# Performance work log

Hardware: AMD Instinct MI355X
Metric: run time of the kernel (lower is better)

## Reference

```python
import jax, jax.numpy as jnp
import numpy as np

B, L, S, DIM, H, DH, DFF = 2, 2048, 2048, 1024, 16, 64, 4096
EPS = 1e-6


def _ln(x, w, b):
    m = jnp.mean(x, axis=-1, keepdims=True)
    v = jnp.mean(jnp.square(x - m), axis=-1, keepdims=True)
    return (x - m) / jnp.sqrt(v + EPS) * w + b


def _mha(q, k, v, mask):
    # q: [B,L,H*DH], k/v: [B,S,H*DH], mask broadcastable to [B,H,L,S], True = masked
    b, l, _ = q.shape
    s = k.shape[1]
    q = q.reshape(b, l, H, DH)
    k = k.reshape(b, s, H, DH)
    v = v.reshape(b, s, H, DH)
    scale = 1.0 / np.sqrt(DH).astype(np.float32)
    attn = jnp.einsum('blhd,bshd->bhls', q, k) * scale
    if mask is not None:
        attn = jnp.where(mask, -jnp.inf, attn)
    attn = jax.nn.softmax(attn, axis=-1)
    out = jnp.einsum('bhls,bshd->blhd', attn, v)
    return out.reshape(b, l, H * DH)


def setup_inputs() -> dict:
    key = jax.random.key(0)
    ks = jax.random.split(key, 12)
    std = 0.02
    inp = {
        'input': jax.random.normal(ks[0], (B, L, DIM), jnp.float32),
        'source': jax.random.normal(ks[1], (B, S, DIM), jnp.float32),
        # source mask: no source positions masked
        'source_mask': jnp.zeros((B, 1, 1, S), bool),
        # causal mask for self-attention (True above diagonal -> masked)
        'mask': jnp.triu(jnp.ones((L, L), bool), 1)[None, None],
        # self-attention
        'ln_self_w': jnp.ones((DIM,), jnp.float32),
        'ln_self_b': jnp.zeros((DIM,), jnp.float32),
        'w_qkv': std * jax.random.normal(ks[2], (DIM, 3 * DIM), jnp.float32),
        'b_qkv': jnp.zeros((3 * DIM,), jnp.float32),
        'w_so': std * jax.random.normal(ks[3], (DIM, DIM), jnp.float32),
        'b_so': jnp.zeros((DIM,), jnp.float32),
        # cross-attention
        'ln_cross_w': jnp.ones((DIM,), jnp.float32),
        'ln_cross_b': jnp.zeros((DIM,), jnp.float32),
        'w_q': std * jax.random.normal(ks[4], (DIM, DIM), jnp.float32),
        'b_q': jnp.zeros((DIM,), jnp.float32),
        'w_kv': std * jax.random.normal(ks[5], (DIM, 2 * DIM), jnp.float32),
        'b_kv': jnp.zeros((2 * DIM,), jnp.float32),
        'w_co': std * jax.random.normal(ks[6], (DIM, DIM), jnp.float32),
        'b_co': jnp.zeros((DIM,), jnp.float32),
        # MLP (1 layer)
        'ln_mlp_w': jnp.ones((DIM,), jnp.float32),
        'ln_mlp_b': jnp.zeros((DIM,), jnp.float32),
        'w_ff1': std * jax.random.normal(ks[7], (DIM, DFF), jnp.float32),
        'b_ff1': jnp.zeros((DFF,), jnp.float32),
        'w_ff2': std * jax.random.normal(ks[8], (DFF, DIM), jnp.float32),
        'b_ff2': jnp.zeros((DIM,), jnp.float32),
    }
    return inp


def reference(input, source, source_mask, mask,
              ln_self_w, ln_self_b, w_qkv, b_qkv, w_so, b_so,
              ln_cross_w, ln_cross_b, w_q, b_q, w_kv, b_kv, w_co, b_co,
              ln_mlp_w, ln_mlp_b, w_ff1, b_ff1, w_ff2, b_ff2):
    x = input
    # self-attention block (pre-LN)
    h = _ln(x, ln_self_w, ln_self_b)
    qkv = h @ w_qkv + b_qkv
    q, k, v = jnp.split(qkv, 3, axis=-1)
    sa = _mha(q, k, v, mask) @ w_so + b_so
    x = x + sa
    # cross-attention block (pre-LN)
    h = _ln(x, ln_cross_w, ln_cross_b)
    q = h @ w_q + b_q
    kv = source @ w_kv + b_kv
    k, v = jnp.split(kv, 2, axis=-1)
    ca = _mha(q, k, v, source_mask) @ w_co + b_co
    x = x + ca
    # feed-forward block (pre-LN), eval mode (no dropout/droppath)
    h = _ln(x, ln_mlp_w, ln_mlp_b)
    ff = jax.nn.gelu(h @ w_ff1 + b_ff1, approximate=False) @ w_ff2 + b_ff2
    x = x + ff
    return x
```

## Files before the change

### kernel.cpp

```cpp
#include <hip/hip_runtime.h>
#include <hip/hip_bf16.h>
#include <math.h>

typedef __bf16 bf16_t;
typedef __bf16 bf16x8 __attribute__((ext_vector_type(8)));
typedef __bf16 bf16x4 __attribute__((ext_vector_type(4)));
typedef float  f32x4  __attribute__((ext_vector_type(4)));

#define DIM   1024
#define NB    2
#define NL    2048
#define NS    2048
#define NH    16
#define NDH   64
#define NDFF  4096

template<int N> struct IC { static constexpr int value = N; };

#define DS_READ_B128(dst, addr) \
    asm volatile("ds_read_b128 %0, %1" : "=v"(dst) : "v"(addr))
#define LGKM0_FENCE() do { \
    asm volatile("s_waitcnt lgkmcnt(0)" ::: "memory"); \
    __builtin_amdgcn_sched_barrier(0); } while (0)

__device__ __forceinline__ bf16x8 ld_bf16x8(const bf16_t* p) {
    return *reinterpret_cast<const bf16x8*>(p);
}

__device__ __forceinline__ void gl_lds16(const bf16_t* g, bf16_t* l) {
    __builtin_amdgcn_global_load_lds(
        (const __attribute__((address_space(1))) void*)g,
        (__attribute__((address_space(3))) void*)l, 16, 0, 0);
}

__device__ __forceinline__ unsigned lds_u32(const bf16_t* p) {
    return (unsigned)(uintptr_t)(__attribute__((address_space(3))) const void*)p;
}

__global__ __launch_bounds__(256)
void wconv_kernel(const float* __restrict__ in, bf16_t* __restrict__ out, int K, int N)
{
    __shared__ float tile[32][33];
    int n0 = blockIdx.x * 32, k0 = blockIdx.y * 32;
    int tx = threadIdx.x & 31, ty = threadIdx.x >> 5;
    #pragma unroll
    for (int j = 0; j < 4; ++j)
        tile[ty + 8*j][tx] = in[(size_t)(k0 + ty + 8*j) * N + n0 + tx];
    __syncthreads();
    #pragma unroll
    for (int j = 0; j < 4; ++j)
        out[(size_t)(n0 + ty + 8*j) * K + k0 + tx] = (bf16_t)tile[tx][ty + 8*j];
}

__global__ __launch_bounds__(256)
void f2b_kernel(const float* __restrict__ in, bf16_t* __restrict__ out)
{
    size_t i = ((size_t)blockIdx.x * 256 + threadIdx.x) * 4;
    float4 v = *reinterpret_cast<const float4*>(in + i);
    bf16x4 o = { (bf16_t)v.x, (bf16_t)v.y, (bf16_t)v.z, (bf16_t)v.w };
    *reinterpret_cast<bf16x4*>(out + i) = o;
}

__global__ __launch_bounds__(256)
void ln_kernel(const float* __restrict__ x, const float* __restrict__ wgt,
               const float* __restrict__ bia, bf16_t* __restrict__ out)
{
    int row = blockIdx.x, tid = threadIdx.x;
    float4 xv = reinterpret_cast<const float4*>(x + (size_t)row * DIM)[tid];
    float s1 = xv.x + xv.y + xv.z + xv.w;
    float s2 = xv.x*xv.x + xv.y*xv.y + xv.z*xv.z + xv.w*xv.w;
    #pragma unroll
    for (int off = 32; off > 0; off >>= 1) {
        s1 += __shfl_xor(s1, off, 64);
        s2 += __shfl_xor(s2, off, 64);
    }
    __shared__ float red[8];
    int w = tid >> 6;
    if ((tid & 63) == 0) { red[w] = s1; red[w + 4] = s2; }
    __syncthreads();
    s1 = red[0] + red[1] + red[2] + red[3];
    s2 = red[4] + red[5] + red[6] + red[7];
    float mean = s1 * (1.0f / DIM);
    float var  = s2 * (1.0f / DIM) - mean * mean;
    float rstd = rsqrtf(var + 1e-6f);
    float4 wv = reinterpret_cast<const float4*>(wgt)[tid];
    float4 bv = reinterpret_cast<const float4*>(bia)[tid];
    bf16x4 o = { (bf16_t)((xv.x - mean) * rstd * wv.x + bv.x),
                 (bf16_t)((xv.y - mean) * rstd * wv.y + bv.y),
                 (bf16_t)((xv.z - mean) * rstd * wv.z + bv.z),
                 (bf16_t)((xv.w - mean) * rstd * wv.w + bv.w) };
    reinterpret_cast<bf16x4*>(out + (size_t)row * DIM)[tid] = o;
}

template<int EPI, int BM, int BN>
__global__ __launch_bounds__(256)
void gemm_kernel(const bf16_t* __restrict__ A, const bf16_t* __restrict__ BT,
                 const float* __restrict__ bias, const float* __restrict__ res,
                 void* __restrict__ out, int M, int N, int K)
{
    constexpr int WM = BM / 2, WN = BN / 2;
    constexpr int AM = WM / 16, AN = WN / 16;
    constexpr int ABE = (BM + BN) * 32;
    constexpr int LPS = (BM + BN) / 64;
    __shared__ __align__(16) bf16_t lds[3 * ABE];

    int tid = threadIdx.x;
    int lane = tid & 63, w = tid >> 6;
    int wr = w >> 1, wc = w & 1;
    int la = lane & 15, lg = lane >> 4;
    int m0 = blockIdx.y * BM, n0 = blockIdx.x * BN;

    f32x4 acc[AM][AN] = {};

    int sr = lane >> 2;
    int sc = ((lane & 3) ^ ((lane >> 3) & 3)) * 8;
    const bf16_t* Ap = A  + (size_t)(m0 + w * (BM / 4) + sr) * K + sc;
    const bf16_t* Bp = BT + (size_t)(n0 + w * (BN / 4) + sr) * K + sc;

    auto stage = [&](int t, int buf) {
        int k0 = t * 32;
        bf16_t* base = &lds[buf * ABE];
        #pragma unroll
        for (int i = 0; i < BM / 64; ++i)
            gl_lds16(Ap + ((size_t)i * 16) * K + k0, base + (w * (BM / 4) + i * 16) * 32);
        #pragma unroll
        for (int i = 0; i < BN / 64; ++i)
            gl_lds16(Bp + ((size_t)i * 16) * K + k0, base + (BM + w * (BN / 4) + i * 16) * 32);
    };

    unsigned ldsb = lds_u32(lds);
    unsigned kla = (la >> 1) & 3;
    unsigned a_base = ldsb + ((wr * WM + la) * 32 + (lg ^ kla) * 8) * 2;
    unsigned b_base = ldsb + (BM * 32 + (wc * WN + la) * 32 + (lg ^ kla) * 8) * 2;

    auto compute = [&](int buf) {
        unsigned dB = (unsigned)(buf * ABE * 2);
        bf16x8 af[AM], bfr[AN];
        #pragma unroll
        for (int mi = 0; mi < AM; ++mi)
            DS_READ_B128(af[mi], a_base + dB + mi * 1024);
        #pragma unroll
        for (int ni = 0; ni < AN; ++ni)
            DS_READ_B128(bfr[ni], b_base + dB + ni * 1024);
        LGKM0_FENCE();
        __builtin_amdgcn_s_setprio(1);
        #pragma unroll
        for (int mi = 0; mi < AM; ++mi)
            #pragma unroll
            for (int ni = 0; ni < AN; ++ni)
                acc[mi][ni] = __builtin_amdgcn_mfma_f32_16x16x32_bf16(
                                  af[mi], bfr[ni], acc[mi][ni], 0, 0, 0);
        __builtin_amdgcn_s_setprio(0);
    };

    int nt = K / 32;
    stage(0, 0);
    stage(1, 1);
    int buf = 0;
    for (int t = 0; t < nt - 1; ++t) {
        asm volatile("s_waitcnt vmcnt(%0)" :: "n"(LPS) : "memory");
        __builtin_amdgcn_s_barrier();
        __builtin_amdgcn_sched_barrier(0);
        if (t + 2 < nt) stage(t + 2, (t + 2) % 3);
        compute(buf);
        buf = (buf == 2) ? 0 : buf + 1;
    }
    asm volatile("s_waitcnt vmcnt(0)" ::: "memory");
    __builtin_amdgcn_s_barrier();
    __builtin_amdgcn_sched_barrier(0);
    compute(buf);

    #pragma unroll
    for (int mi = 0; mi < AM; ++mi) {
        #pragma unroll
        for (int ni = 0; ni < AN; ++ni) {
            #pragma unroll
            for (int i = 0; i < 4; ++i) {
                int row = m0 + wr * WM + mi * 16 + lg * 4 + i;
                int col = n0 + wc * WN + ni * 16 + la;
                float v = acc[mi][ni][i] + bias[col];
                if (EPI == 1) v = 0.5f * v * (1.0f + erff(v * 0.70710678118f));
                if (EPI == 2)
                    ((float*)out)[(size_t)row * N + col] = res[(size_t)row * N + col] + v;
                else
                    ((bf16_t*)out)[(size_t)row * N + col] = (bf16_t)v;
            }
        }
    }
}

template<int EPI>
__global__ __launch_bounds__(512, 2)
void gemm256d_kernel(const bf16_t* __restrict__ A, const bf16_t* __restrict__ BT,
                     const float* __restrict__ bias, void* __restrict__ out,
                     int M, int N, int K, int nbx)
{
    constexpr int DBE = 16384;
    __shared__ __align__(16) bf16_t lds[4 * DBE];

    int tid = threadIdx.x;
    int lane = tid & 63, w = tid >> 6;
    int wr = w >> 2, wc = w & 3;
    int la = lane & 15, lg = lane >> 4;

    int nwg = gridDim.x, bid = blockIdx.x;
    int swz = (bid & 7) * (nwg >> 3) + (bid >> 3);
    int m0 = (swz / nbx) * 256, n0 = (swz % nbx) * 256;

    f32x4 acc[8][4] = {};

    int sr = lane >> 2;
    int sc = ((lane & 3) ^ ((lane >> 3) & 3)) * 8;
    const bf16_t* Ap = A  + (size_t)(m0 + w * 16 + sr) * K + sc;
    const bf16_t* Bp = BT + (size_t)(n0 + w * 16 + sr) * K + sc;

    auto stage = [&](int t) {
        int k0 = t * 32;
        bf16_t* base = &lds[(t & 3) * DBE];
        gl_lds16(Ap + k0,                     base + w * 512);
        gl_lds16(Ap + (size_t)128 * K + k0,   base + 4096 + w * 512);
        gl_lds16(Bp + k0,                     base + 8192 + w * 512);
        gl_lds16(Bp + (size_t)128 * K + k0,   base + 12288 + w * 512);
    };

    unsigned ldsb = lds_u32(lds);
    unsigned kla = (la >> 1) & 3;
    unsigned a_base = ldsb + ((wr * 128 + la) * 32 + (lg ^ kla) * 8) * 2;
    unsigned b_base = ldsb + (8192 + (wc * 64 + la) * 32 + (lg ^ kla) * 8) * 2;

    int nt = K / 32;

    auto ktile = [&](int kt, auto vmc, bool do_stage) {
        if (do_stage) stage(kt + 3);
        asm volatile("s_waitcnt vmcnt(%0)" :: "n"(decltype(vmc)::value) : "memory");
        __builtin_amdgcn_s_barrier();
        __builtin_amdgcn_sched_barrier(0);
        unsigned dB = (unsigned)((kt & 3) * (DBE * 2));
        bf16x8 af[4], af2[4], bfr[4];
        #pragma unroll
        for (int mi = 0; mi < 4; ++mi)
            DS_READ_B128(af[mi], a_base + dB + mi * 1024);
        #pragma unroll
        for (int ni = 0; ni < 4; ++ni)
            DS_READ_B128(bfr[ni], b_base + dB + ni * 1024);
        LGKM0_FENCE();
        __builtin_amdgcn_s_setprio(1);
        #pragma unroll
        for (int mi = 0; mi < 4; ++mi)
            #pragma unroll
            for (int ni = 0; ni < 4; ++ni)
                acc[mi][ni] = __builtin_amdgcn_mfma_f32_16x16x32_bf16(
                                  af[mi], bfr[ni], acc[mi][ni], 0, 0, 0);
        __builtin_amdgcn_s_setprio(0);
        #pragma unroll
        for (int mi = 0; mi < 4; ++mi)
            DS_READ_B128(af2[mi], a_base + dB + (4 + mi) * 1024);
        LGKM0_FENCE();
        __builtin_amdgcn_s_setprio(1);
        #pragma unroll
        for (int mi = 0; mi < 4; ++mi)
            #pragma unroll
            for (int ni = 0; ni < 4; ++ni)
                acc[4 + mi][ni] = __builtin_amdgcn_mfma_f32_16x16x32_bf16(
                                      af2[mi], bfr[ni], acc[4 + mi][ni], 0, 0, 0);
        __builtin_amdgcn_s_setprio(0);
        __builtin_amdgcn_s_barrier();
        __builtin_amdgcn_sched_barrier(0);
    };

    stage(0); stage(1); stage(2);
    for (int kt = 0; kt < nt - 3; ++kt) ktile(kt, IC<12>{}, true);
    ktile(nt - 3, IC<8>{}, false);
    ktile(nt - 2, IC<4>{}, false);
    ktile(nt - 1, IC<0>{}, false);

    #pragma unroll
    for (int mi = 0; mi < 8; ++mi) {
        #pragma unroll
        for (int ni = 0; ni < 4; ++ni) {
            #pragma unroll
            for (int i = 0; i < 4; ++i) {
                int row = m0 + wr * 128 + mi * 16 + lg * 4 + i;
                int col = n0 + wc * 64 + ni * 16 + la;
                float v = acc[mi][ni][i] + bias[col];
                if (EPI == 1) v = 0.5f * v * (1.0f + erff(v * 0.70710678118f));
                ((bf16_t*)out)[(size_t)row * N + col] = (bf16_t)v;
            }
        }
    }
}

template<bool CAUSAL>
__global__ __launch_bounds__(256)
void attn_kernel(const bf16_t* __restrict__ Q, int qs,
                 const bf16_t* __restrict__ Kp, int ks,
                 const bf16_t* __restrict__ Vp, int vs,
                 bf16_t* __restrict__ O, int os, int L, int S)
{
    __shared__ __align__(16) bf16_t Ks[64 * 64];
    __shared__ __align__(16) bf16_t Vt[64 * 64];
    __shared__ __align__(16) bf16_t Ps[4][16 * 64];

    int tid = threadIdx.x, lane = tid & 63, w = tid >> 6;
    int la = lane & 15, lg = lane >> 4;
    int qtile = (CAUSAL ? (gridDim.x - 1 - blockIdx.x) : blockIdx.x) * 64;
    int b = blockIdx.y >> 4, h = blockIdx.y & 15;

    const bf16_t* qb = Q  + (size_t)(b * L) * qs + h * 64;
    const bf16_t* kb = Kp + (size_t)(b * S) * ks + h * 64;
    const bf16_t* vb = Vp + (size_t)(b * S) * vs + h * 64;
    bf16_t*       ob = O  + (size_t)(b * L) * os + h * 64;

    int qrow = qtile + w * 16 + la;
    bf16x8 qf0 = ld_bf16x8(qb + (size_t)qrow * qs + lg * 8);
    bf16x8 qf1 = ld_bf16x8(qb + (size_t)qrow * qs + 32 + lg * 8);
    #pragma unroll
    for (int j = 0; j < 8; ++j) { qf0[j] = qf0[j] * (bf16_t)0.125f; qf1[j] = qf1[j] * (bf16_t)0.125f; }

    f32x4 zero = {0.f, 0.f, 0.f, 0.f};
    f32x4 o[4];
    #pragma unroll
    for (int dt = 0; dt < 4; ++dt) o[dt] = zero;
    float lpart[4] = {0.f, 0.f, 0.f, 0.f};

    int rk  = tid >> 3;
    int ck8 = tid & 7;
    int sv0   = tid & 31;
    int dbase = (tid >> 5) * 8;
    int r7 = la & 7;

    int n_full = (CAUSAL ? qtile : S) / 64;
    int nit = n_full + (CAUSAL ? 1 : 0);

    bf16x8 kr0 = ld_bf16x8(kb + (size_t)rk * ks + ck8 * 8);
    bf16x8 kr1 = ld_bf16x8(kb + (size_t)(rk + 32) * ks + ck8 * 8);
    bf16x8 vr0 = ld_bf16x8(vb + (size_t)sv0 * vs + dbase);
    bf16x8 vr1 = ld_bf16x8(vb + (size_t)(sv0 + 32) * vs + dbase);

    for (int it = 0; it < nit; ++it) {
        int s0 = it * 64;
        bool diag = CAUSAL && (it == n_full);

        __syncthreads();
        *reinterpret_cast<bf16x8*>(&Ks[rk * 64 + ((ck8 ^ (rk & 7)) * 8)]) = kr0;
        *reinterpret_cast<bf16x8*>(&Ks[(rk + 32) * 64 + ((ck8 ^ (rk & 7)) * 8)]) = kr1;
        #pragma unroll
        for (int j = 0; j < 8; ++j) {
            Vt[(dbase + j) * 64 + (sv0 ^ (j << 3))]        = vr0[j];
            Vt[(dbase + j) * 64 + ((sv0 + 32) ^ (j << 3))] = vr1[j];
        }
        __syncthreads();

        if (it + 1 < nit) {
            int s1 = s0 + 64;
            kr0 = ld_bf16x8(kb + (size_t)(s1 + rk) * ks + ck8 * 8);
            kr1 = ld_bf16x8(kb + (size_t)(s1 + rk + 32) * ks + ck8 * 8);
            vr0 = ld_bf16x8(vb + (size_t)(s1 + sv0) * vs + dbase);
            vr1 = ld_bf16x8(vb + (size_t)(s1 + sv0 + 32) * vs + dbase);
        }

        f32x4 sf[4];
        #pragma unroll
        for (int ct = 0; ct < 4; ++ct) {
            const bf16_t* kr = &Ks[(ct * 16 + la) * 64];
            bf16x8 k0 = ld_bf16x8(kr + ((lg ^ r7) * 8));
            bf16x8 k1 = ld_bf16x8(kr + (((4 + lg) ^ r7) * 8));
            f32x4 z = zero;
            z = __builtin_amdgcn_mfma_f32_16x16x32_bf16(qf0, k0, z, 0, 0, 0);
            z = __builtin_amdgcn_mfma_f32_16x16x32_bf16(qf1, k1, z, 0, 0, 0);
            sf[ct] = z;
        }

        #pragma unroll
        for (int ct = 0; ct < 4; ++ct) {
            #pragma unroll
            for (int i = 0; i < 4; ++i) {
                float p = __expf(sf[ct][i]);
                if (diag) {
                    int sg = s0 + ct * 16 + la;
                    int qg = qtile + w * 16 + lg * 4 + i;
                    if (sg > qg) p = 0.f;
                }
                lpart[i] += p;
                int row = lg * 4 + i;
                Ps[w][row * 64 + ((ct * 16 + la) ^ ((row & 7) << 3))] = (bf16_t)p;
            }
        }

        bf16x8 pa0 = ld_bf16x8(&Ps[w][la * 64 + ((lg ^ r7) * 8)]);
        bf16x8 pa1 = ld_bf16x8(&Ps[w][la * 64 + (((4 + lg) ^ r7) * 8)]);
        #pragma unroll
        for (int dt = 0; dt < 4; ++dt) {
            const bf16_t* vr = &Vt[(dt * 16 + la) * 64];
            bf16x8 v0 = ld_bf16x8(vr + ((lg ^ r7) * 8));
            bf16x8 v1 = ld_bf16x8(vr + (((4 + lg) ^ r7) * 8));
            o[dt] = __builtin_amdgcn_mfma_f32_16x16x32_bf16(pa0, v0, o[dt], 0, 0, 0);
            o[dt] = __builtin_amdgcn_mfma_f32_16x16x32_bf16(pa1, v1, o[dt], 0, 0, 0);
        }
    }

    #pragma unroll
    for (int off = 1; off < 16; off <<= 1)
        #pragma unroll
        for (int i = 0; i < 4; ++i)
            lpart[i] += __shfl_xor(lpart[i], off, 64);

    #pragma unroll
    for (int dt = 0; dt < 4; ++dt)
        #pragma unroll
        for (int i = 0; i < 4; ++i) {
            int row = qtile + w * 16 + lg * 4 + i;
            float val = o[dt][i] / lpart[i];
            ob[(size_t)row * os + dt * 16 + la] = (bf16_t)val;
        }
}

extern "C" void kernel_launch(void* const* d_in, const int* in_sizes, int n_in,
                              void* d_out, int out_size, void* d_ws, size_t ws_size,
                              hipStream_t stream)
{
    const float* input     = (const float*)d_in[0];
    const float* source    = (const float*)d_in[1];
    const float* ln_self_w = (const float*)d_in[4];
    const float* ln_self_b = (const float*)d_in[5];
    const float* w_qkv     = (const float*)d_in[6];
    const float* b_qkv     = (const float*)d_in[7];
    const float* w_so      = (const float*)d_in[8];
    const float* b_so      = (const float*)d_in[9];
    const float* ln_cross_w= (const float*)d_in[10];
    const float* ln_cross_b= (const float*)d_in[11];
    const float* w_q       = (const float*)d_in[12];
    const float* b_q       = (const float*)d_in[13];
    const float* w_kv      = (const float*)d_in[14];
    const float* b_kv      = (const float*)d_in[15];
    const float* w_co      = (const float*)d_in[16];
    const float* b_co      = (const float*)d_in[17];
    const float* ln_mlp_w  = (const float*)d_in[18];
    const float* ln_mlp_b  = (const float*)d_in[19];
    const float* w_ff1     = (const float*)d_in[20];
    const float* b_ff1     = (const float*)d_in[21];
    const float* w_ff2     = (const float*)d_in[22];
    const float* b_ff2     = (const float*)d_in[23];

    const int M = NB * NL;

    char* ws = (char*)d_ws;
    size_t off = 0;
    auto alloc = [&](size_t bytes) { char* p = ws + off; off += (bytes + 255) & ~(size_t)255; return p; };

    bf16_t* wT_qkv = (bf16_t*)alloc((size_t)3072 * 1024 * 2);
    bf16_t* wT_so  = (bf16_t*)alloc((size_t)1024 * 1024 * 2);
    bf16_t* wT_q   = (bf16_t*)alloc((size_t)1024 * 1024 * 2);
    bf16_t* wT_kv  = (bf16_t*)alloc((size_t)2048 * 1024 * 2);
    bf16_t* wT_co  = (bf16_t*)alloc((size_t)1024 * 1024 * 2);
    bf16_t* wT_ff1 = (bf16_t*)alloc((size_t)4096 * 1024 * 2);
    bf16_t* wT_ff2 = (bf16_t*)alloc((size_t)1024 * 4096 * 2);
    bf16_t* srcb   = (bf16_t*)alloc((size_t)M * 1024 * 2);
    bf16_t* hbuf   = (bf16_t*)alloc((size_t)M * 1024 * 2);
    bf16_t* qkvb   = (bf16_t*)alloc((size_t)M * 3072 * 2);
    bf16_t* attnb  = (bf16_t*)alloc((size_t)M * 1024 * 2);
    bf16_t* qcb    = (bf16_t*)alloc((size_t)M * 1024 * 2);
    bf16_t* kvcb   = (bf16_t*)alloc((size_t)M * 2048 * 2);
    float*  xbuf   = (float*) alloc((size_t)M * 1024 * 4);
    bf16_t* ff1b   = (bf16_t*)alloc((size_t)M * 4096 * 2);
    (void)ws_size; (void)n_in; (void)in_sizes; (void)out_size;

    wconv_kernel<<<dim3(3072/32, 1024/32), 256, 0, stream>>>(w_qkv, wT_qkv, 1024, 3072);
    wconv_kernel<<<dim3(1024/32, 1024/32), 256, 0, stream>>>(w_so,  wT_so,  1024, 1024);
    wconv_kernel<<<dim3(1024/32, 1024/32), 256, 0, stream>>>(w_q,   wT_q,   1024, 1024);
    wconv_kernel<<<dim3(2048/32, 1024/32), 256, 0, stream>>>(w_kv,  wT_kv,  1024, 2048);
    wconv_kernel<<<dim3(1024/32, 1024/32), 256, 0, stream>>>(w_co,  wT_co,  1024, 1024);
    wconv_kernel<<<dim3(4096/32, 1024/32), 256, 0, stream>>>(w_ff1, wT_ff1, 1024, 4096);
    wconv_kernel<<<dim3(1024/32, 4096/32), 256, 0, stream>>>(w_ff2, wT_ff2, 4096, 1024);
    f2b_kernel<<<(M * 1024) / (256 * 4), 256, 0, stream>>>(source, srcb);

    ln_kernel<<<M, 256, 0, stream>>>(input, ln_self_w, ln_self_b, hbuf);
    gemm_kernel<0,128,128><<<dim3(3072/128, M/128), 256, 0, stream>>>(hbuf, wT_qkv, b_qkv, nullptr, qkvb, M, 3072, 1024);
    attn_kernel<true><<<dim3(NL/64, NB*NH), 256, 0, stream>>>(qkvb, 3072, qkvb + 1024, 3072, qkvb + 2048, 3072,
                                                              attnb, 1024, NL, NL);
    gemm_kernel<2,128,64><<<dim3(1024/64, M/128), 256, 0, stream>>>(attnb, wT_so, b_so, input, xbuf, M, 1024, 1024);

    ln_kernel<<<M, 256, 0, stream>>>(xbuf, ln_cross_w, ln_cross_b, hbuf);
    gemm_kernel<0,128,64><<<dim3(1024/64, M/128), 256, 0, stream>>>(hbuf, wT_q, b_q, nullptr, qcb, M, 1024, 1024);
    gemm_kernel<0,128,128><<<dim3(2048/128, M/128), 256, 0, stream>>>(srcb, wT_kv, b_kv, nullptr, kvcb, M, 2048, 1024);
    attn_kernel<false><<<dim3(NL/64, NB*NH), 256, 0, stream>>>(qcb, 1024, kvcb, 2048, kvcb + 1024, 2048,
                                                               attnb, 1024, NL, NS);
    gemm_kernel<2,128,64><<<dim3(1024/64, M/128), 256, 0, stream>>>(attnb, wT_co, b_co, xbuf, xbuf, M, 1024, 1024);

    ln_kernel<<<M, 256, 0, stream>>>(xbuf, ln_mlp_w, ln_mlp_b, hbuf);
    gemm256d_kernel<1><<<dim3((4096/256) * (M/256)), 512, 0, stream>>>(hbuf, wT_ff1, b_ff1, ff1b, M, 4096, 1024, 4096/256);
    gemm_kernel<2,128,64><<<dim3(1024/64, M/128), 256, 0, stream>>>(ff1b, wT_ff2, b_ff2, xbuf, d_out, M, 1024, 4096);
}
```

Measured before the change: 467.9 us.

## Split 256-tile GEMM into staggered A/B phases, use it for QKV/KV and split-K FF2

The 256x256 GEMM's k-loop is split into two half-phases, each issuing its own half of the next stage's global-to-LDS loads, so memory traffic is interleaved with MFMA work. The kernel is generalised with leading dimensions and a K-offset per grid.y, and is now used for the QKV and cross-KV projections. FF2 runs as a 4-way split-K into fp32 partial buffers, followed by a reduction kernel that adds bias and residual. This aims at better occupancy and load overlap for the N=1024, K=4096 GEMM, at the cost of extra partial-sum memory traffic. The partials reuse the source bf16 buffer, which must be large enough and no longer needed at that point.

```diff
diff --git a/kernel.cpp b/kernel.cpp
--- a/kernel.cpp
+++ b/kernel.cpp
@@ -14,8 +14,6 @@
 #define NH    16
 #define NDH   64
 #define NDFF  4096
-
-template<int N> struct IC { static constexpr int value = N; };
 
 #define DS_READ_B128(dst, addr) \
     asm volatile("ds_read_b128 %0, %1" : "=v"(dst) : "v"(addr))
@@ -191,9 +189,10 @@
 
 template<int EPI>
 __global__ __launch_bounds__(512, 2)
-void gemm256d_kernel(const bf16_t* __restrict__ A, const bf16_t* __restrict__ BT,
+void gemm256f_kernel(const bf16_t* __restrict__ A, int lda,
+                     const bf16_t* __restrict__ BT, int ldb,
                      const float* __restrict__ bias, void* __restrict__ out,
-                     int M, int N, int K, int nbx)
+                     int M, int N, int Kc, int nbx)
 {
     constexpr int DBE = 16384;
     __shared__ __align__(16) bf16_t lds[4 * DBE];
@@ -206,21 +205,26 @@
     int nwg = gridDim.x, bid = blockIdx.x;
     int swz = (bid & 7) * (nwg >> 3) + (bid >> 3);
     int m0 = (swz / nbx) * 256, n0 = (swz % nbx) * 256;
+    int koff = blockIdx.y * Kc;
 
     f32x4 acc[8][4] = {};
 
     int sr = lane >> 2;
     int sc = ((lane & 3) ^ ((lane >> 3) & 3)) * 8;
-    const bf16_t* Ap = A  + (size_t)(m0 + w * 16 + sr) * K + sc;
-    const bf16_t* Bp = BT + (size_t)(n0 + w * 16 + sr) * K + sc;
-
-    auto stage = [&](int t) {
+    const bf16_t* Ap = A  + (size_t)(m0 + w * 16 + sr) * lda + koff + sc;
+    const bf16_t* Bp = BT + (size_t)(n0 + w * 16 + sr) * ldb + koff + sc;
+
+    auto stageA = [&](int t) {
         int k0 = t * 32;
-        bf16_t* base = &lds[(t & 3) * DBE];
-        gl_lds16(Ap + k0,                     base + w * 512);
-        gl_lds16(Ap + (size_t)128 * K + k0,   base + 4096 + w * 512);
-        gl_lds16(Bp + k0,                     base + 8192 + w * 512);
-        gl_lds16(Bp + (size_t)128 * K + k0,   base + 12288 + w * 512);
+        bf16_t* b = &lds[(t & 3) * DBE];
+        gl_lds16(Ap + k0,                       b + w * 512);
+        gl_lds16(Ap + (size_t)128 * lda + k0,   b + 4096 + w * 512);
+    };
+    auto stageB = [&](int t) {
+        int k0 = t * 32;
+        bf16_t* b = &lds[(t & 3) * DBE];
+        gl_lds16(Bp + k0,                       b + 8192 + w * 512);
+        gl_lds16(Bp + (size_t)128 * ldb + k0,   b + 12288 + w * 512);
     };
 
     unsigned ldsb = lds_u32(lds);
@@ -228,21 +232,20 @@
     unsigned a_base = ldsb + ((wr * 128 + la) * 32 + (lg ^ kla) * 8) * 2;
     unsigned b_base = ldsb + (8192 + (wc * 64 + la) * 32 + (lg ^ kla) * 8) * 2;
 
-    int nt = K / 32;
-
-    auto ktile = [&](int kt, auto vmc, bool do_stage) {
-        if (do_stage) stage(kt + 3);
-        asm volatile("s_waitcnt vmcnt(%0)" :: "n"(decltype(vmc)::value) : "memory");
-        __builtin_amdgcn_s_barrier();
-        __builtin_amdgcn_sched_barrier(0);
+    int nt = Kc / 32;
+    bf16x8 bfr[4];
+
+    auto phA = [&](int kt, bool st) {
         unsigned dB = (unsigned)((kt & 3) * (DBE * 2));
-        bf16x8 af[4], af2[4], bfr[4];
+        bf16x8 af[4];
         #pragma unroll
         for (int mi = 0; mi < 4; ++mi)
             DS_READ_B128(af[mi], a_base + dB + mi * 1024);
         #pragma unroll
         for (int ni = 0; ni < 4; ++ni)
             DS_READ_B128(bfr[ni], b_base + dB + ni * 1024);
+        if (st) stageA(kt + 3);
+        __builtin_amdgcn_s_barrier();
         LGKM0_FENCE();
         __builtin_amdgcn_s_setprio(1);
         #pragma unroll
@@ -252,9 +255,15 @@
                 acc[mi][ni] = __builtin_amdgcn_mfma_f32_16x16x32_bf16(
                                   af[mi], bfr[ni], acc[mi][ni], 0, 0, 0);
         __builtin_amdgcn_s_setprio(0);
+    };
+    auto phB = [&](int kt, bool st) {
+        unsigned dB = (unsigned)((kt & 3) * (DBE * 2));
+        bf16x8 af[4];
         #pragma unroll
         for (int mi = 0; mi < 4; ++mi)
-            DS_READ_B128(af2[mi], a_base + dB + (4 + mi) * 1024);
+            DS_READ_B128(af[mi], a_base + dB + 4096 + mi * 1024);
+        if (st) stageB(kt + 3);
+        __builtin_amdgcn_s_barrier();
         LGKM0_FENCE();
         __builtin_amdgcn_s_setprio(1);
         #pragma unroll
@@ -262,18 +271,32 @@
             #pragma unroll
             for (int ni = 0; ni < 4; ++ni)
                 acc[4 + mi][ni] = __builtin_amdgcn_mfma_f32_16x16x32_bf16(
-                                      af2[mi], bfr[ni], acc[4 + mi][ni], 0, 0, 0);
+                                      af[mi], bfr[ni], acc[4 + mi][ni], 0, 0, 0);
         __builtin_amdgcn_s_setprio(0);
+    };
+
+    stageA(0); stageB(0); stageA(1); stageB(1); stageA(2); stageB(2);
+    asm volatile("s_waitcnt vmcnt(8)" ::: "memory");
+    __builtin_amdgcn_s_barrier();
+    __builtin_amdgcn_sched_barrier(0);
+
+    for (int kt = 0; kt < nt - 3; ++kt) {
+        phA(kt, true); phB(kt, true);
+        asm volatile("s_waitcnt vmcnt(8)" ::: "memory");
         __builtin_amdgcn_s_barrier();
         __builtin_amdgcn_sched_barrier(0);
-    };
-
-    stage(0); stage(1); stage(2);
-    for (int kt = 0; kt < nt - 3; ++kt) ktile(kt, IC<12>{}, true);
-    ktile(nt - 3, IC<8>{}, false);
-    ktile(nt - 2, IC<4>{}, false);
-    ktile(nt - 1, IC<0>{}, false);
-
+    }
+    phA(nt - 3, false); phB(nt - 3, false);
+    asm volatile("s_waitcnt vmcnt(4)" ::: "memory");
+    __builtin_amdgcn_s_barrier();
+    __builtin_amdgcn_sched_barrier(0);
+    phA(nt - 2, false); phB(nt - 2, false);
+    asm volatile("s_waitcnt vmcnt(0)" ::: "memory");
+    __builtin_amdgcn_s_barrier();
+    __builtin_amdgcn_sched_barrier(0);
+    phA(nt - 1, false); phB(nt - 1, false);
+
+    float* po = (float*)out + (size_t)blockIdx.y * M * N;
     #pragma unroll
     for (int mi = 0; mi < 8; ++mi) {
         #pragma unroll
@@ -282,12 +305,37 @@
             for (int i = 0; i < 4; ++i) {
                 int row = m0 + wr * 128 + mi * 16 + lg * 4 + i;
                 int col = n0 + wc * 64 + ni * 16 + la;
-                float v = acc[mi][ni][i] + bias[col];
-                if (EPI == 1) v = 0.5f * v * (1.0f + erff(v * 0.70710678118f));
-                ((bf16_t*)out)[(size_t)row * N + col] = (bf16_t)v;
+                float v = acc[mi][ni][i];
+                if (EPI == 3) {
+                    po[(size_t)row * N + col] = v;
+                } else {
+                    v += bias[col];
+                    if (EPI == 1) v = 0.5f * v * (1.0f + erff(v * 0.70710678118f));
+                    ((bf16_t*)out)[(size_t)row * N + col] = (bf16_t)v;
+                }
             }
         }
     }
+}
+
+__global__ __launch_bounds__(256)
+void ff2red_kernel(const float* __restrict__ part, const float* __restrict__ res,
+                   const float* __restrict__ bias, float* __restrict__ out)
+{
+    size_t i = ((size_t)blockIdx.x * 256 + threadIdx.x) * 4;
+    const size_t CH = (size_t)4096 * 1024;
+    float4 a0 = *reinterpret_cast<const float4*>(part + i);
+    float4 a1 = *reinterpret_cast<const float4*>(part + CH + i);
+    float4 a2 = *reinterpret_cast<const float4*>(part + 2 * CH + i);
+    float4 a3 = *reinterpret_cast<const float4*>(part + 3 * CH + i);
+    float4 rv = *reinterpret_cast<const float4*>(res + i);
+    float4 bv = *reinterpret_cast<const float4*>(bias + (i & 1023));
+    float4 o;
+    o.x = rv.x + bv.x + ((a0.x + a1.x) + (a2.x + a3.x));
+    o.y = rv.y + bv.y + ((a0.y + a1.y) + (a2.y + a3.y));
+    o.z = rv.z + bv.z + ((a0.z + a1.z) + (a2.z + a3.z));
+    o.w = rv.w + bv.w + ((a0.w + a1.w) + (a2.w + a3.w));
+    *reinterpret_cast<float4*>(out + i) = o;
 }
 
 template<bool CAUSAL>
@@ -465,6 +513,8 @@
     bf16_t* ff1b   = (bf16_t*)alloc((size_t)M * 4096 * 2);
     (void)ws_size; (void)n_in; (void)in_sizes; (void)out_size;
 
+    float* ff2part = (float*)srcb;
+
     wconv_kernel<<<dim3(3072/32, 1024/32), 256, 0, stream>>>(w_qkv, wT_qkv, 1024, 3072);
     wconv_kernel<<<dim3(1024/32, 1024/32), 256, 0, stream>>>(w_so,  wT_so,  1024, 1024);
     wconv_kernel<<<dim3(1024/32, 1024/32), 256, 0, stream>>>(w_q,   wT_q,   1024, 1024);
@@ -475,19 +525,24 @@
     f2b_kernel<<<(M * 1024) / (256 * 4), 256, 0, stream>>>(source, srcb);
 
     ln_kernel<<<M, 256, 0, stream>>>(input, ln_self_w, ln_self_b, hbuf);
-    gemm_kernel<0,128,128><<<dim3(3072/128, M/128), 256, 0, stream>>>(hbuf, wT_qkv, b_qkv, nullptr, qkvb, M, 3072, 1024);
+    gemm256f_kernel<0><<<dim3(192, 1), 512, 0, stream>>>(hbuf, 1024, wT_qkv, 1024,
+                                                         b_qkv, qkvb, M, 3072, 1024, 12);
     attn_kernel<true><<<dim3(NL/64, NB*NH), 256, 0, stream>>>(qkvb, 3072, qkvb + 1024, 3072, qkvb + 2048, 3072,
                                                               attnb, 1024, NL, NL);
     gemm_kernel<2,128,64><<<dim3(1024/64, M/128), 256, 0, stream>>>(attnb, wT_so, b_so, input, xbuf, M, 1024, 1024);
 
     ln_kernel<<<M, 256, 0, stream>>>(xbuf, ln_cross_w, ln_cross_b, hbuf);
     gemm_kernel<0,128,64><<<dim3(1024/64, M/128), 256, 0, stream>>>(hbuf, wT_q, b_q, nullptr, qcb, M, 1024, 1024);
-    gemm_kernel<0,128,128><<<dim3(2048/128, M/128), 256, 0, stream>>>(srcb, wT_kv, b_kv, nullptr, kvcb, M, 2048, 1024);
+    gemm256f_kernel<0><<<dim3(128, 1), 512, 0, stream>>>(srcb, 1024, wT_kv, 1024,
+                                                         b_kv, kvcb, M, 2048, 1024, 8);
     attn_kernel<false><<<dim3(NL/64, NB*NH), 256, 0, stream>>>(qcb, 1024, kvcb, 2048, kvcb + 1024, 2048,
                                                                attnb, 1024, NL, NS);
     gemm_kernel<2,128,64><<<dim3(1024/64, M/128), 256, 0, stream>>>(attnb, wT_co, b_co, xbuf, xbuf, M, 1024, 1024);
 
     ln_kernel<<<M, 256, 0, stream>>>(xbuf, ln_mlp_w, ln_mlp_b, hbuf);
-    gemm256d_kernel<1><<<dim3((4096/256) * (M/256)), 512, 0, stream>>>(hbuf, wT_ff1, b_ff1, ff1b, M, 4096, 1024, 4096/256);
-    gemm_kernel<2,128,64><<<dim3(1024/64, M/128), 256, 0, stream>>>(ff1b, wT_ff2, b_ff2, xbuf, d_out, M, 1024, 4096);
-}
+    gemm256f_kernel<1><<<dim3(256, 1), 512, 0, stream>>>(hbuf, 1024, wT_ff1, 1024,
+                                                         b_ff1, ff1b, M, 4096, 1024, 16);
+    gemm256f_kernel<3><<<dim3(64, 4), 512, 0, stream>>>(ff1b, 4096, wT_ff2, 4096,
+                                                        nullptr, ff2part, M, 1024, 1024, 4);
+    ff2red_kernel<<<(M * 1024) / (256 * 4), 256, 0, stream>>>(ff2part, xbuf, b_ff2, (float*)d_out);
+}
```

Result: slower. 489.3 us (+4.6%).
